# Kernel optimization log

Measured on AMD Instinct MI355X. Metric: run time of the kernel, lower is better.

The kernel has to match this reference:

```python
import jax, jax.numpy as jnp
import numpy as np

N_NODES = 20000
N_EDGES = 320000
N_GRAPHS = 512
HEADS1 = 10
C1 = 78   # per-head out channels of gcn1
C2 = 100  # out channels of gcn2 (heads=1)
NEG_SLOPE = 0.2


def setup_inputs() -> dict:
    key = jax.random.key(0)
    ks = jax.random.split(key, 16)
    glorot = lambda k, shp: jax.random.normal(k, shp, jnp.float32) * np.sqrt(2.0 / (shp[0] + shp[-1]))
    x = jax.random.normal(ks[0], (N_NODES, 78), jnp.float32)
    edge_index = jax.random.randint(ks[1], (2, N_EDGES), 0, N_NODES, jnp.int64)
    batch = jnp.sort(jax.random.randint(ks[2], (N_NODES,), 0, N_GRAPHS, jnp.int64))
    return {
        "x": x,
        "edge_index": edge_index,
        "batch": batch,
        "num_graphs": N_GRAPHS,
        "W1": glorot(ks[3], (78, HEADS1 * C1)),
        "a_src1": glorot(ks[4], (HEADS1, C1)),
        "a_dst1": glorot(ks[5], (HEADS1, C1)),
        "b1": jnp.zeros((HEADS1 * C1,), jnp.float32),
        "W2": glorot(ks[6], (HEADS1 * C1, C2)),
        "a_src2": glorot(ks[7], (1, C2)),
        "a_dst2": glorot(ks[8], (1, C2)),
        "b2": jnp.zeros((C2,), jnp.float32),
        "Wg": glorot(ks[9], (C2, C2)),
        "bg": jnp.zeros((C2,), jnp.float32),
    }


def gat_conv(x, src, dst, W, a_src, a_dst, b, heads, out_ch):
    """PyG-style GATConv (concat=True, add_self_loops already applied, eval mode)."""
    N = x.shape[0]
    h = (x @ W).reshape(N, heads, out_ch)          # [N,H,C]
    alpha_s = jnp.einsum('nhc,hc->nh', h, a_src)   # [N,H]
    alpha_d = jnp.einsum('nhc,hc->nh', h, a_dst)
    e = jax.nn.leaky_relu(alpha_s[src] + alpha_d[dst], NEG_SLOPE)  # [E,H]
    # segment softmax over destination nodes
    m = jax.ops.segment_max(e, dst, num_segments=N)                # [N,H]
    e = jnp.exp(e - m[dst])
    denom = jax.ops.segment_sum(e, dst, num_segments=N)
    alpha = e / (denom[dst] + 1e-16)                               # [E,H]
    out = jax.ops.segment_sum(h[src] * alpha[:, :, None], dst, num_segments=N)
    return out.reshape(N, heads * out_ch) + b


def reference(x, edge_index, batch, num_graphs, W1, a_src1, a_dst1, b1,
              W2, a_src2, a_dst2, b2, Wg, bg):
    N = x.shape[0]
    # add self loops (PyG GATConv default)
    loops = jnp.arange(N, dtype=edge_index.dtype)
    src = jnp.concatenate([edge_index[0], loops])
    dst = jnp.concatenate([edge_index[1], loops])
    h = gat_conv(x, src, dst, W1, a_src1, a_dst1, b1, HEADS1, C1)   # [N,780]
    h = jax.nn.elu(h)
    h = gat_conv(h, src, dst, W2, a_src2, a_dst2, b2, 1, C2)        # [N,100]
    h = jax.nn.relu(h)
    g = jax.ops.segment_max(h, batch, num_segments=num_graphs)      # [G,100] global max pool
    g = jax.nn.relu(g @ Wg + bg)
    return g
```

## Files before the change

kernel.cpp:

```cpp
#include <hip/hip_runtime.h>
#include <hip/hip_bf16.h>

#define N_NODES  20000
#define N_EDGES  320000
#define E_TOT    (N_EDGES + N_NODES)
#define N_GRAPHS 512
#define H1 10
#define C1 78
#define F1 780
#define C2 100
#define NEG_SLOPE 0.2f
#define KSPLIT 5
#define K1PAD 96
#define K2PAD 800
#define K2CHUNK 160
#define AP1 104
#define AP2 40
#define HP 12

typedef short bf16x8 __attribute__((ext_vector_type(8)));
typedef float f32x4 __attribute__((ext_vector_type(4)));
typedef unsigned short ushort_t;

__device__ __forceinline__ float bf_lo(unsigned int u) { return __uint_as_float(u << 16); }
__device__ __forceinline__ float bf_hi(unsigned int u) { return __uint_as_float(u & 0xFFFF0000u); }
__device__ __forceinline__ ushort_t f2b(float v) {
  __hip_bfloat16 b = __float2bfloat16(v);
  return *reinterpret_cast<ushort_t*>(&b);
}
__device__ __forceinline__ float lrelu(float v) { return (v > 0.f) ? v : NEG_SLOPE * v; }


__global__ void k_count(const int* __restrict__ ei, int* __restrict__ cnt) {
  int e = blockIdx.x * blockDim.x + threadIdx.x;
  if (e >= E_TOT) return;
  int dst = (e < N_EDGES) ? ei[N_EDGES + e] : (e - N_EDGES);
  atomicAdd(&cnt[dst], 1);
}

__global__ __launch_bounds__(1024) void k_scan(const int* __restrict__ cnt,
                                               int* __restrict__ offs, int n) {
  const int PER = 20;
  int t = threadIdx.x;
  int lane = t & 63, wv = t >> 6;
  int base = t * PER;
  int loc[PER];
  int run = 0;
#pragma unroll
  for (int k = 0; k < PER; k++) {
    int idx = base + k;
    int v = (idx < n) ? cnt[idx] : 0;
    run += v;
    loc[k] = run;
  }
  int total = run;
  int sc = total;
#pragma unroll
  for (int o = 1; o < 64; o <<= 1) {
    int u = __shfl_up(sc, o);
    if (lane >= o) sc += u;
  }
  __shared__ int ws[16];
  if (lane == 63) ws[wv] = sc;
  __syncthreads();
  if (t == 0) {
    int r = 0;
#pragma unroll
    for (int i = 0; i < 16; i++) { int v = ws[i]; ws[i] = r; r += v; }
  }
  __syncthreads();
  int excl = ws[wv] + sc - total;
#pragma unroll
  for (int k = 0; k < PER; k++) {
    int idx = base + k;
    if (idx < n) offs[idx + 1] = excl + loc[k];
  }
  if (t == 0) offs[0] = 0;
}

__global__ void k_scatter(const int* __restrict__ ei, const int* __restrict__ offs,
                          int* __restrict__ cursor, int* __restrict__ srcs,
                          int* __restrict__ dsts) {
  int e = blockIdx.x * blockDim.x + threadIdx.x;
  if (e >= E_TOT) return;
  int src, dst;
  if (e < N_EDGES) { src = ei[e]; dst = ei[N_EDGES + e]; }
  else             { src = dst = e - N_EDGES; }
  int pos = offs[dst] + atomicAdd(&cursor[dst], 1);
  srcs[pos] = src;
  dsts[pos] = dst;
}


#define PR0 (2 * H1 * C1)
#define PR1 (H1 * 80 * K1PAD)
#define PR2 (112 * K2PAD)
#define PR3 (N_NODES * (K2PAD - F1))
#define PR4 (N_NODES * 40)

__global__ void k_prep(const float* __restrict__ W1, const float* __restrict__ a_src,
                       const float* __restrict__ a_dst, const float* __restrict__ W2,
                       const float* __restrict__ x,
                       float* __restrict__ Vs, float* __restrict__ Vd,
                       ushort_t* __restrict__ W1t, ushort_t* __restrict__ W2t,
                       ushort_t* __restrict__ hab, ushort_t* __restrict__ xbf) {
  int t = blockIdx.x * blockDim.x + threadIdx.x;
  if (t < PR0) {
    int which = (t >= H1 * C1) ? 1 : 0;
    int r = t - which * H1 * C1;
    int h = r / C1, k = r - h * C1;
    const float* a = which ? a_dst : a_src;
    float s = 0.f;
    for (int c = 0; c < C1; c++) s += W1[(size_t)k * F1 + h * C1 + c] * a[h * C1 + c];
    (which ? Vd : Vs)[h * C1 + k] = s;
    return;
  }
  t -= PR0;
  if (t < PR1) {
    int h = t / (80 * K1PAD);
    int rem = t - h * 80 * K1PAD;
    int c = rem / K1PAD, k = rem - c * K1PAD;
    float v = (c < C1 && k < C1) ? W1[(size_t)k * F1 + h * C1 + c] : 0.f;
    W1t[t] = f2b(v);
    return;
  }
  t -= PR1;
  if (t < PR2) {
    int c = t / K2PAD, k = t - c * K2PAD;
    float v = (c < C2 && k < F1) ? W2[(size_t)k * C2 + c] : 0.f;
    W2t[t] = f2b(v);
    return;
  }
  t -= PR2;
  if (t < PR3) {
    int n = t / (K2PAD - F1), j = t - n * (K2PAD - F1);
    hab[(size_t)n * K2PAD + F1 + j] = 0;
    return;
  }
  t -= PR3;
  if (t < PR4) {
    int n = t / 40, c2 = t - n * 40;
    ushort2 o;
    if (c2 < 39) { o.x = f2b(x[(size_t)n * C1 + 2 * c2]); o.y = f2b(x[(size_t)n * C1 + 2 * c2 + 1]); }
    else         { o.x = 0; o.y = 0; }
    *(ushort2*)(xbf + (size_t)n * 80 + 2 * c2) = o;
  }
}


__global__ __launch_bounds__(256) void k_alpha1x(const float* __restrict__ x,
                                                 const float* __restrict__ Vs,
                                                 const float* __restrict__ Vd,
                                                 float* __restrict__ asb,
                                                 float* __restrict__ adb) {
  __shared__ float sVs[H1 * C1], sVd[H1 * C1];
  for (int i = threadIdx.x; i < H1 * C1; i += 256) { sVs[i] = Vs[i]; sVd[i] = Vd[i]; }
  __syncthreads();
  int t = blockIdx.x * 256 + threadIdx.x;
  if (t >= N_NODES * H1) return;
  int n = t / H1, h = t - n * H1;
  const float2* row = (const float2*)(x + (size_t)n * C1);
  const float2* vs2 = (const float2*)(sVs + h * C1);
  const float2* vd2 = (const float2*)(sVd + h * C1);
  float s0 = 0.f, s1 = 0.f;
#pragma unroll 13
  for (int i = 0; i < C1 / 2; i++) {
    float2 v = row[i];
    float2 a = vs2[i];
    float2 b = vd2[i];
    s0 += v.x * a.x + v.y * a.y;
    s1 += v.x * b.x + v.y * b.y;
  }
  asb[(size_t)n * HP + h] = s0;
  adb[(size_t)n * HP + h] = s1;
}


__global__ void k_ex1(const float* __restrict__ asb, const float* __restrict__ adb,
                      const int* __restrict__ srcs, const int* __restrict__ dsts,
                      unsigned int* __restrict__ ex1) {
  int e = blockIdx.x * blockDim.x + threadIdx.x;
  if (e > E_TOT) return;
  unsigned int* o = ex1 + (size_t)e * 5;
  if (e == E_TOT) {
#pragma unroll
    for (int q = 0; q < 5; q++) o[q] = 0u;
    return;
  }
  int s = srcs[e], d = dsts[e];
  const float* pa = asb + (size_t)s * HP;
  const float* pd = adb + (size_t)d * HP;
  float4 a0 = *(const float4*)pa, a1 = *(const float4*)(pa + 4);
  float2 a2 = *(const float2*)(pa + 8);
  float4 d0 = *(const float4*)pd, d1 = *(const float4*)(pd + 4);
  float2 d2 = *(const float2*)(pd + 8);
  float r[10];
  r[0] = __expf(lrelu(a0.x + d0.x)); r[1] = __expf(lrelu(a0.y + d0.y));
  r[2] = __expf(lrelu(a0.z + d0.z)); r[3] = __expf(lrelu(a0.w + d0.w));
  r[4] = __expf(lrelu(a1.x + d1.x)); r[5] = __expf(lrelu(a1.y + d1.y));
  r[6] = __expf(lrelu(a1.z + d1.z)); r[7] = __expf(lrelu(a1.w + d1.w));
  r[8] = __expf(lrelu(a2.x + d2.x)); r[9] = __expf(lrelu(a2.y + d2.y));
#pragma unroll
  for (int q = 0; q < 5; q++)
    o[q] = (unsigned int)f2b(r[2 * q]) | ((unsigned int)f2b(r[2 * q + 1]) << 16);
}


__global__ __launch_bounds__(256) void k_aggv4(const ushort_t* __restrict__ xbf,
                                               const unsigned int* __restrict__ ex1,
                                               const int* __restrict__ offs,
                                               const int* __restrict__ srcs,
                                               ushort_t* __restrict__ xb) {
  int wid = (blockIdx.x * 256 + threadIdx.x) >> 6;
  int lane = threadIdx.x & 63;
  if (wid >= N_NODES) return;
  int n = wid;
  int beg = offs[n], deg = offs[n + 1] - beg;

  float acc[H1][2] = {};
  float sum[H1] = {};

  for (int j = 0; j < deg; j += 2) {
    int e0 = beg + j;
    int s0 = srcs[e0];
    bool v1 = (j + 1) < deg;
    int e1 = v1 ? e0 + 1 : E_TOT;
    int s1 = v1 ? srcs[e0 + 1] : s0;
    unsigned int w0[5], w1[5];
#pragma unroll
    for (int q = 0; q < 5; q++) { w0[q] = ex1[(size_t)e0 * 5 + q]; w1[q] = ex1[(size_t)e1 * 5 + q]; }
    unsigned int xv0 = 0, xv1 = 0;
    if (lane < 39) {
      xv0 = *(const unsigned int*)(xbf + (size_t)s0 * 80 + 2 * lane);
      xv1 = *(const unsigned int*)(xbf + (size_t)s1 * 80 + 2 * lane);
    }
    float xl0 = bf_lo(xv0), xh0 = bf_hi(xv0);
    float xl1 = bf_lo(xv1), xh1 = bf_hi(xv1);
#pragma unroll
    for (int h = 0; h < H1; h++) {
      float p0 = (h & 1) ? bf_hi(w0[h >> 1]) : bf_lo(w0[h >> 1]);
      float p1 = (h & 1) ? bf_hi(w1[h >> 1]) : bf_lo(w1[h >> 1]);
      acc[h][0] += p0 * xl0 + p1 * xl1;
      acc[h][1] += p0 * xh0 + p1 * xh1;
      sum[h] += p0 + p1;
    }
  }

  if (lane < 48) {
    int colu = (lane < 39) ? 2 * lane : C1 + 2 * (lane - 39);
#pragma unroll
    for (int h = 0; h < H1; h++) {
      float iv = 1.f / (sum[h] + 1e-16f);
      ushort2 o;
      if (lane < 39) { o.x = f2b(acc[h][0] * iv); o.y = f2b(acc[h][1] * iv); }
      else           { o.x = 0; o.y = 0; }
      *(ushort2*)(xb + ((size_t)h * N_NODES + n) * K1PAD + colu) = o;
    }
  }
}


__global__ __launch_bounds__(256) void k_bgemm_m(const ushort_t* __restrict__ xb,
                                                 const ushort_t* __restrict__ W1t,
                                                 const float* __restrict__ b1,
                                                 ushort_t* __restrict__ hab) {
  __shared__ ushort_t sA[64 * AP1];
  __shared__ ushort_t sB[80 * AP1];
  int h = blockIdx.y;
  int m0 = blockIdx.x * 64;
  int tid = threadIdx.x;

  for (int i = tid; i < 64 * 12; i += 256) {
    int r = i / 12, cx = i - r * 12;
    uint4 v = make_uint4(0, 0, 0, 0);
    int m = m0 + r;
    if (m < N_NODES) v = *(const uint4*)(xb + ((size_t)h * N_NODES + m) * K1PAD + cx * 8);
    *(uint4*)(sA + r * AP1 + cx * 8) = v;
  }
  for (int i = tid; i < 80 * 12; i += 256) {
    int c = i / 12, cx = i - c * 12;
    uint4 v = *(const uint4*)(W1t + ((size_t)h * 80 + c) * K1PAD + cx * 8);
    *(uint4*)(sB + c * AP1 + cx * 8) = v;
  }
  __syncthreads();

  int w = tid >> 6, l = tid & 63;
  int rb = l & 15, g = l >> 4;
  f32x4 acc[5] = {};
  const ushort_t* pa = sA + (w * 16 + rb) * AP1 + g * 8;
#pragma unroll
  for (int k0 = 0; k0 < K1PAD; k0 += 32) {
    bf16x8 a = *(const bf16x8*)(pa + k0);
#pragma unroll
    for (int ct = 0; ct < 5; ct++) {
      bf16x8 b = *(const bf16x8*)(sB + (ct * 16 + rb) * AP1 + k0 + g * 8);
      acc[ct] = __builtin_amdgcn_mfma_f32_16x16x32_bf16(a, b, acc[ct], 0, 0, 0);
    }
  }

  int mrow = m0 + w * 16 + g * 4;
#pragma unroll
  for (int ct = 0; ct < 5; ct++) {
    int col = ct * 16 + rb;
    if (col >= C1) continue;
    float bias = b1[h * C1 + col];
#pragma unroll
    for (int r = 0; r < 4; r++) {
      int m = mrow + r;
      if (m >= N_NODES) continue;
      float v = acc[ct][r] + bias;
      v = (v > 0.f) ? v : (__expf(v) - 1.f);
      hab[(size_t)m * K2PAD + h * C1 + col] = f2b(v);
    }
  }
}


__global__ __launch_bounds__(256) void k_gemm2m(const ushort_t* __restrict__ hab,
                                                const ushort_t* __restrict__ W2t,
                                                float* __restrict__ part) {
  __shared__ ushort_t sA[64 * AP2];
  __shared__ ushort_t sB[112 * AP2];
  int m0 = blockIdx.x * 64;
  int kz = blockIdx.y * K2CHUNK;
  int tid = threadIdx.x;
  int w = tid >> 6, l = tid & 63;
  int rb = l & 15, g = l >> 4;
  f32x4 acc[7] = {};

  for (int ks = 0; ks < K2CHUNK; ks += 32) {
    int kbase = kz + ks;
    {
      int r = tid >> 2, cx = tid & 3;
      uint4 v = make_uint4(0, 0, 0, 0);
      int m = m0 + r;
      if (m < N_NODES) v = *(const uint4*)(hab + (size_t)m * K2PAD + kbase + cx * 8);
      *(uint4*)(sA + r * AP2 + cx * 8) = v;
    }
    for (int i = tid; i < 112 * 4; i += 256) {
      int c = i >> 2, cx = i & 3;
      uint4 v = *(const uint4*)(W2t + (size_t)c * K2PAD + kbase + cx * 8);
      *(uint4*)(sB + c * AP2 + cx * 8) = v;
    }
    __syncthreads();
    bf16x8 a = *(const bf16x8*)(sA + (w * 16 + rb) * AP2 + g * 8);
#pragma unroll
    for (int ct = 0; ct < 7; ct++) {
      bf16x8 b = *(const bf16x8*)(sB + (ct * 16 + rb) * AP2 + g * 8);
      acc[ct] = __builtin_amdgcn_mfma_f32_16x16x32_bf16(a, b, acc[ct], 0, 0, 0);
    }
    __syncthreads();
  }

  float* P = part + (size_t)blockIdx.y * N_NODES * C2;
  int mrow = m0 + w * 16 + g * 4;
#pragma unroll
  for (int ct = 0; ct < 7; ct++) {
    int col = ct * 16 + rb;
    if (col >= C2) continue;
#pragma unroll
    for (int r = 0; r < 4; r++) {
      int m = mrow + r;
      if (m < N_NODES) P[(size_t)m * C2 + col] = acc[ct][r];
    }
  }
}


__global__ __launch_bounds__(256) void k_redalpha(const float* __restrict__ part,
                                                  const float* __restrict__ a_src,
                                                  const float* __restrict__ a_dst,
                                                  ushort_t* __restrict__ z2b,
                                                  float* __restrict__ as2,
                                                  float* __restrict__ ad2) {
  int wid = (blockIdx.x * 256 + threadIdx.x) >> 6;
  int lane = threadIdx.x & 63;
  if (wid >= N_NODES) return;
  float ps = 0.f, pd = 0.f;
  if (lane < C2 / 2) {
    float2 s = make_float2(0.f, 0.f);
#pragma unroll
    for (int c = 0; c < KSPLIT; c++) {
      float2 v = *(const float2*)(part + (size_t)c * N_NODES * C2 + (size_t)wid * C2 + 2 * lane);
      s.x += v.x; s.y += v.y;
    }
    ushort2 o; o.x = f2b(s.x); o.y = f2b(s.y);
    *(ushort2*)(z2b + (size_t)wid * C2 + 2 * lane) = o;
    ps = s.x * a_src[2 * lane] + s.y * a_src[2 * lane + 1];
    pd = s.x * a_dst[2 * lane] + s.y * a_dst[2 * lane + 1];
  }
#pragma unroll
  for (int o = 32; o; o >>= 1) { ps += __shfl_xor(ps, o); pd += __shfl_xor(pd, o); }
  if (lane == 0) { as2[wid] = ps; ad2[wid] = pd; }
}


__global__ void k_ex2(const float* __restrict__ as2, const float* __restrict__ ad2,
                      const int* __restrict__ srcs, const int* __restrict__ dsts,
                      float* __restrict__ ex2) {
  int e = blockIdx.x * blockDim.x + threadIdx.x;
  if (e > E_TOT) return;
  if (e == E_TOT) { ex2[e] = 0.f; return; }
  float v = as2[srcs[e]] + ad2[dsts[e]];
  ex2[e] = __expf(lrelu(v));
}


__global__ __launch_bounds__(256) void k_gat2v3(const ushort_t* __restrict__ z2b,
                                                const float* __restrict__ ex2,
                                                const int* __restrict__ offs,
                                                const int* __restrict__ srcs,
                                                const float* __restrict__ b2,
                                                const int* __restrict__ batch,
                                                unsigned int* __restrict__ pool) {
  int wid = (blockIdx.x * 256 + threadIdx.x) >> 6;
  int lane = threadIdx.x & 63;
  if (wid >= N_NODES) return;
  int n = wid;
  int beg = offs[n], deg = offs[n + 1] - beg;
  const unsigned int* zrow = (const unsigned int*)z2b;

  float acc0 = 0.f, acc1 = 0.f, sum = 0.f;

  for (int j = 0; j < deg; j += 8) {
    int ej[8], sj[8];
#pragma unroll
    for (int q = 0; q < 8; q++) {
      int jj = j + q;
      bool v = jj < deg;
      ej[q] = v ? beg + jj : E_TOT;
      sj[q] = srcs[v ? beg + jj : beg];
    }
    float p[8];
#pragma unroll
    for (int q = 0; q < 8; q++) p[q] = ex2[ej[q]];
    unsigned int z[8] = {0, 0, 0, 0, 0, 0, 0, 0};
    if (lane < C2 / 2) {
#pragma unroll
      for (int q = 0; q < 8; q++) z[q] = zrow[(size_t)sj[q] * (C2 / 2) + lane];
    }
#pragma unroll
    for (int q = 0; q < 8; q++) {
      acc0 += p[q] * bf_lo(z[q]);
      acc1 += p[q] * bf_hi(z[q]);
      sum += p[q];
    }
  }

  if (lane < C2 / 2) {
    float iv = 1.f / (sum + 1e-16f);
    float v0 = fmaxf(acc0 * iv + b2[2 * lane], 0.f);
    float v1 = fmaxf(acc1 * iv + b2[2 * lane + 1], 0.f);
    int g = batch[n];
    atomicMax(&pool[g * C2 + 2 * lane], __float_as_uint(v0));
    atomicMax(&pool[g * C2 + 2 * lane + 1], __float_as_uint(v1));
  }
}


__global__ __launch_bounds__(128) void k_head(const float* __restrict__ pool,
                                              const float* __restrict__ Wg,
                                              const float* __restrict__ bg,
                                              float* __restrict__ out) {
  __shared__ float row[C2];
  int g = blockIdx.x;
  if (threadIdx.x < C2) row[threadIdx.x] = pool[g * C2 + threadIdx.x];
  __syncthreads();
  int c = threadIdx.x;
  if (c < C2) {
    float acc = bg[c];
    for (int k = 0; k < C2; k++) acc += row[k] * Wg[k * C2 + c];
    out[g * C2 + c] = fmaxf(acc, 0.f);
  }
}


extern "C" void kernel_launch(void* const* d_in, const int* in_sizes, int n_in,
                              void* d_out, int out_size, void* d_ws, size_t ws_size,
                              hipStream_t stream) {
  const float* x      = (const float*)d_in[0];
  const int*   ei     = (const int*)d_in[1];
  const int*   batch  = (const int*)d_in[2];
  const float* W1     = (const float*)d_in[4];
  const float* a_src1 = (const float*)d_in[5];
  const float* a_dst1 = (const float*)d_in[6];
  const float* b1     = (const float*)d_in[7];
  const float* W2     = (const float*)d_in[8];
  const float* a_src2 = (const float*)d_in[9];
  const float* a_dst2 = (const float*)d_in[10];
  const float* b2     = (const float*)d_in[11];
  const float* Wg     = (const float*)d_in[12];
  const float* bg     = (const float*)d_in[13];
  float* out = (float*)d_out;

  char* w = (char*)d_ws;
  size_t off = 0;
  auto alloc = [&](size_t bytes) -> void* {
    void* p = w + off;
    off += (bytes + 255) & ~(size_t)255;
    return p;
  };

  ushort_t* xb  = (ushort_t*)alloc((size_t)H1 * N_NODES * K1PAD * 2);
  ushort_t* hab = (ushort_t*)alloc((size_t)N_NODES * K2PAD * 2);
  float* part   = (float*)alloc((size_t)KSPLIT * N_NODES * C2 * 4);
  float* asb    = (float*)alloc((size_t)N_NODES * HP * 4);
  float* adb    = (float*)alloc((size_t)N_NODES * HP * 4);
  unsigned int* ex1 = (unsigned int*)alloc((size_t)(E_TOT + 1) * 5 * 4);
  ushort_t* xbf = (ushort_t*)alloc((size_t)N_NODES * 80 * 2);
  float* Vs     = (float*)alloc((size_t)H1 * C1 * 4);
  float* Vd     = (float*)alloc((size_t)H1 * C1 * 4);
  ushort_t* W1t = (ushort_t*)alloc((size_t)H1 * 80 * K1PAD * 2);
  ushort_t* W2t = (ushort_t*)alloc((size_t)112 * K2PAD * 2);
  int* cnt           = (int*)alloc((size_t)N_NODES * 4);
  int* cursor        = (int*)alloc((size_t)N_NODES * 4);
  unsigned int* pool = (unsigned int*)alloc((size_t)N_GRAPHS * C2 * 4);
  size_t zspan = (size_t)((char*)(pool + (size_t)N_GRAPHS * C2) - (char*)cnt);
  int* offs   = (int*)alloc((size_t)(N_NODES + 1) * 4);
  int* srcs   = (int*)alloc((size_t)E_TOT * 4);
  int* dsts   = (int*)alloc((size_t)E_TOT * 4);

  float* as2    = (float*)xb;
  float* ad2    = as2 + N_NODES;
  ushort_t* z2b = (ushort_t*)(ad2 + N_NODES);
  float* ex2    = (float*)(z2b + (size_t)N_NODES * C2);

  hipMemsetAsync(cnt, 0, zspan, stream);

  k_count<<<(E_TOT + 255) / 256, 256, 0, stream>>>(ei, cnt);
  k_scan<<<1, 1024, 0, stream>>>(cnt, offs, N_NODES);
  k_scatter<<<(E_TOT + 255) / 256, 256, 0, stream>>>(ei, offs, cursor, srcs, dsts);

  k_prep<<<(PR0 + PR1 + PR2 + PR3 + PR4 + 255) / 256, 256, 0, stream>>>(
      W1, a_src1, a_dst1, W2, x, Vs, Vd, W1t, W2t, hab, xbf);
  k_alpha1x<<<(N_NODES * H1 + 255) / 256, 256, 0, stream>>>(x, Vs, Vd, asb, adb);
  k_ex1<<<(E_TOT + 1 + 255) / 256, 256, 0, stream>>>(asb, adb, srcs, dsts, ex1);
  k_aggv4<<<(N_NODES + 3) / 4, 256, 0, stream>>>(xbf, ex1, offs, srcs, xb);
  k_bgemm_m<<<dim3((N_NODES + 63) / 64, H1), 256, 0, stream>>>(xb, W1t, b1, hab);

  k_gemm2m<<<dim3((N_NODES + 63) / 64, KSPLIT), 256, 0, stream>>>(hab, W2t, part);
  k_redalpha<<<(N_NODES + 3) / 4, 256, 0, stream>>>(part, a_src2, a_dst2, z2b, as2, ad2);
  k_ex2<<<(E_TOT + 1 + 255) / 256, 256, 0, stream>>>(as2, ad2, srcs, dsts, ex2);
  k_gat2v3<<<(N_NODES + 3) / 4, 256, 0, stream>>>(z2b, ex2, offs, srcs, b2, batch, pool);
  k_head<<<N_GRAPHS, 128, 0, stream>>>((const float*)pool, Wg, bg, out);
}
```

Baseline: 280.8 us.

## Use fp16 packed dot2 and head-major edge weights in layer-1 aggregation

Layer-1 aggregation now stores node features and per-edge exp scores in fp16 instead of bf16. The exp scores move to a head-major [H, E] layout so each head's weights for an edge pair load as one aligned 32-bit word. The inner loop uses v_dot2_f32_f16 (fdot2) to accumulate two edges per instruction for the weighted sums and the normaliser, with bitmasks handling odd edge-range boundaries. This replaces the scalar bf16-unpack and FMA work and the padded sentinel edge. It trades bf16 range for fp16 range on unnormalised exp values, so large logits could overflow to inf, and inf multiplied by a zero mask gives NaN.

After: 275.6 us. About the same (-1.8%).

```diff
diff --git a/kernel.cpp b/kernel.cpp
--- a/kernel.cpp
+++ b/kernel.cpp
@@ -20,6 +20,7 @@
 
 typedef short bf16x8 __attribute__((ext_vector_type(8)));
 typedef float f32x4 __attribute__((ext_vector_type(4)));
+typedef _Float16 half2v __attribute__((ext_vector_type(2)));
 typedef unsigned short ushort_t;
 
 __device__ __forceinline__ float bf_lo(unsigned int u) { return __uint_as_float(u << 16); }
@@ -28,7 +29,16 @@
   __hip_bfloat16 b = __float2bfloat16(v);
   return *reinterpret_cast<ushort_t*>(&b);
 }
+__device__ __forceinline__ ushort_t f2h(float v) {
+  _Float16 h = (_Float16)v;
+  return *reinterpret_cast<ushort_t*>(&h);
+}
 __device__ __forceinline__ float lrelu(float v) { return (v > 0.f) ? v : NEG_SLOPE * v; }
+__device__ __forceinline__ float dot2h(unsigned int a, unsigned int b, float c) {
+  union { unsigned int u; half2v v; } A, B;
+  A.u = a; B.u = b;
+  return __builtin_amdgcn_fdot2(A.v, B.v, c, false);
+}
 
 
 __global__ void k_count(const int* __restrict__ ei, int* __restrict__ cnt) {
@@ -103,7 +113,7 @@
                        const float* __restrict__ x,
                        float* __restrict__ Vs, float* __restrict__ Vd,
                        ushort_t* __restrict__ W1t, ushort_t* __restrict__ W2t,
-                       ushort_t* __restrict__ hab, ushort_t* __restrict__ xbf) {
+                       ushort_t* __restrict__ hab, ushort_t* __restrict__ xhf) {
   int t = blockIdx.x * blockDim.x + threadIdx.x;
   if (t < PR0) {
     int which = (t >= H1 * C1) ? 1 : 0;
@@ -141,9 +151,9 @@
   if (t < PR4) {
     int n = t / 40, c2 = t - n * 40;
     ushort2 o;
-    if (c2 < 39) { o.x = f2b(x[(size_t)n * C1 + 2 * c2]); o.y = f2b(x[(size_t)n * C1 + 2 * c2 + 1]); }
+    if (c2 < 39) { o.x = f2h(x[(size_t)n * C1 + 2 * c2]); o.y = f2h(x[(size_t)n * C1 + 2 * c2 + 1]); }
     else         { o.x = 0; o.y = 0; }
-    *(ushort2*)(xbf + (size_t)n * 80 + 2 * c2) = o;
+    *(ushort2*)(xhf + (size_t)n * 80 + 2 * c2) = o;
   }
 }
 
@@ -178,15 +188,9 @@
 
 __global__ void k_ex1(const float* __restrict__ asb, const float* __restrict__ adb,
                       const int* __restrict__ srcs, const int* __restrict__ dsts,
-                      unsigned int* __restrict__ ex1) {
+                      ushort_t* __restrict__ ex1t) {
   int e = blockIdx.x * blockDim.x + threadIdx.x;
-  if (e > E_TOT) return;
-  unsigned int* o = ex1 + (size_t)e * 5;
-  if (e == E_TOT) {
-#pragma unroll
-    for (int q = 0; q < 5; q++) o[q] = 0u;
-    return;
-  }
+  if (e >= E_TOT) return;
   int s = srcs[e], d = dsts[e];
   const float* pa = asb + (size_t)s * HP;
   const float* pd = adb + (size_t)d * HP;
@@ -201,13 +205,12 @@
   r[6] = __expf(lrelu(a1.z + d1.z)); r[7] = __expf(lrelu(a1.w + d1.w));
   r[8] = __expf(lrelu(a2.x + d2.x)); r[9] = __expf(lrelu(a2.y + d2.y));
 #pragma unroll
-  for (int q = 0; q < 5; q++)
-    o[q] = (unsigned int)f2b(r[2 * q]) | ((unsigned int)f2b(r[2 * q + 1]) << 16);
-}
-
-
-__global__ __launch_bounds__(256) void k_aggv4(const ushort_t* __restrict__ xbf,
-                                               const unsigned int* __restrict__ ex1,
+  for (int h = 0; h < H1; h++) ex1t[(size_t)h * E_TOT + e] = f2h(r[h]);
+}
+
+
+__global__ __launch_bounds__(256) void k_aggv5(const ushort_t* __restrict__ xhf,
+                                               const ushort_t* __restrict__ ex1t,
                                                const int* __restrict__ offs,
                                                const int* __restrict__ srcs,
                                                ushort_t* __restrict__ xb) {
@@ -215,34 +218,34 @@
   int lane = threadIdx.x & 63;
   if (wid >= N_NODES) return;
   int n = wid;
-  int beg = offs[n], deg = offs[n + 1] - beg;
-
-  float acc[H1][2] = {};
-  float sum[H1] = {};
-
-  for (int j = 0; j < deg; j += 2) {
-    int e0 = beg + j;
-    int s0 = srcs[e0];
-    bool v1 = (j + 1) < deg;
-    int e1 = v1 ? e0 + 1 : E_TOT;
-    int s1 = v1 ? srcs[e0 + 1] : s0;
-    unsigned int w0[5], w1[5];
-#pragma unroll
-    for (int q = 0; q < 5; q++) { w0[q] = ex1[(size_t)e0 * 5 + q]; w1[q] = ex1[(size_t)e1 * 5 + q]; }
+  int beg = __builtin_amdgcn_readfirstlane(offs[n]);
+  int end = __builtin_amdgcn_readfirstlane(offs[n + 1]);
+
+  float acc0[H1] = {}, acc1[H1] = {}, sum[H1] = {};
+  const unsigned int ONES = 0x3C003C00u;
+
+  for (int e0 = beg & ~1; e0 < end; e0 += 2) {
+    unsigned int m = 0xFFFFFFFFu;
+    if (e0 < beg) m &= 0xFFFF0000u;
+    if (e0 + 1 >= end) m &= 0x0000FFFFu;
+    int s0 = srcs[e0], s1 = srcs[e0 + 1];
+    unsigned int w[H1];
+#pragma unroll
+    for (int h = 0; h < H1; h++)
+      w[h] = *(const unsigned int*)(ex1t + (size_t)h * E_TOT + e0);
     unsigned int xv0 = 0, xv1 = 0;
     if (lane < 39) {
-      xv0 = *(const unsigned int*)(xbf + (size_t)s0 * 80 + 2 * lane);
-      xv1 = *(const unsigned int*)(xbf + (size_t)s1 * 80 + 2 * lane);
-    }
-    float xl0 = bf_lo(xv0), xh0 = bf_hi(xv0);
-    float xl1 = bf_lo(xv1), xh1 = bf_hi(xv1);
+      xv0 = *(const unsigned int*)(xhf + (size_t)s0 * 80 + 2 * lane);
+      xv1 = *(const unsigned int*)(xhf + (size_t)s1 * 80 + 2 * lane);
+    }
+    unsigned int xA = __builtin_amdgcn_perm(xv1, xv0, 0x05040100u) & m;
+    unsigned int xB = __builtin_amdgcn_perm(xv1, xv0, 0x07060302u) & m;
+    unsigned int on = ONES & m;
 #pragma unroll
     for (int h = 0; h < H1; h++) {
-      float p0 = (h & 1) ? bf_hi(w0[h >> 1]) : bf_lo(w0[h >> 1]);
-      float p1 = (h & 1) ? bf_hi(w1[h >> 1]) : bf_lo(w1[h >> 1]);
-      acc[h][0] += p0 * xl0 + p1 * xl1;
-      acc[h][1] += p0 * xh0 + p1 * xh1;
-      sum[h] += p0 + p1;
+      acc0[h] = dot2h(w[h], xA, acc0[h]);
+      acc1[h] = dot2h(w[h], xB, acc1[h]);
+      sum[h]  = dot2h(w[h], on, sum[h]);
     }
   }
 
@@ -252,7 +255,7 @@
     for (int h = 0; h < H1; h++) {
       float iv = 1.f / (sum[h] + 1e-16f);
       ushort2 o;
-      if (lane < 39) { o.x = f2b(acc[h][0] * iv); o.y = f2b(acc[h][1] * iv); }
+      if (lane < 39) { o.x = f2b(acc0[h] * iv); o.y = f2b(acc1[h] * iv); }
       else           { o.x = 0; o.y = 0; }
       *(ushort2*)(xb + ((size_t)h * N_NODES + n) * K1PAD + colu) = o;
     }
@@ -501,17 +504,17 @@
     return p;
   };
 
-  ushort_t* xb  = (ushort_t*)alloc((size_t)H1 * N_NODES * K1PAD * 2);
-  ushort_t* hab = (ushort_t*)alloc((size_t)N_NODES * K2PAD * 2);
-  float* part   = (float*)alloc((size_t)KSPLIT * N_NODES * C2 * 4);
-  float* asb    = (float*)alloc((size_t)N_NODES * HP * 4);
-  float* adb    = (float*)alloc((size_t)N_NODES * HP * 4);
-  unsigned int* ex1 = (unsigned int*)alloc((size_t)(E_TOT + 1) * 5 * 4);
-  ushort_t* xbf = (ushort_t*)alloc((size_t)N_NODES * 80 * 2);
-  float* Vs     = (float*)alloc((size_t)H1 * C1 * 4);
-  float* Vd     = (float*)alloc((size_t)H1 * C1 * 4);
-  ushort_t* W1t = (ushort_t*)alloc((size_t)H1 * 80 * K1PAD * 2);
-  ushort_t* W2t = (ushort_t*)alloc((size_t)112 * K2PAD * 2);
+  ushort_t* xb   = (ushort_t*)alloc((size_t)H1 * N_NODES * K1PAD * 2);
+  ushort_t* hab  = (ushort_t*)alloc((size_t)N_NODES * K2PAD * 2);
+  float* part    = (float*)alloc((size_t)KSPLIT * N_NODES * C2 * 4);
+  float* asb     = (float*)alloc((size_t)N_NODES * HP * 4);
+  float* adb     = (float*)alloc((size_t)N_NODES * HP * 4);
+  ushort_t* ex1t = (ushort_t*)alloc((size_t)H1 * E_TOT * 2);
+  ushort_t* xhf  = (ushort_t*)alloc((size_t)N_NODES * 80 * 2);
+  float* Vs      = (float*)alloc((size_t)H1 * C1 * 4);
+  float* Vd      = (float*)alloc((size_t)H1 * C1 * 4);
+  ushort_t* W1t  = (ushort_t*)alloc((size_t)H1 * 80 * K1PAD * 2);
+  ushort_t* W2t  = (ushort_t*)alloc((size_t)112 * K2PAD * 2);
   int* cnt           = (int*)alloc((size_t)N_NODES * 4);
   int* cursor        = (int*)alloc((size_t)N_NODES * 4);
   unsigned int* pool = (unsigned int*)alloc((size_t)N_GRAPHS * C2 * 4);
@@ -532,10 +535,10 @@
   k_scatter<<<(E_TOT + 255) / 256, 256, 0, stream>>>(ei, offs, cursor, srcs, dsts);
 
   k_prep<<<(PR0 + PR1 + PR2 + PR3 + PR4 + 255) / 256, 256, 0, stream>>>(
-      W1, a_src1, a_dst1, W2, x, Vs, Vd, W1t, W2t, hab, xbf);
+      W1, a_src1, a_dst1, W2, x, Vs, Vd, W1t, W2t, hab, xhf);
   k_alpha1x<<<(N_NODES * H1 + 255) / 256, 256, 0, stream>>>(x, Vs, Vd, asb, adb);
-  k_ex1<<<(E_TOT + 1 + 255) / 256, 256, 0, stream>>>(asb, adb, srcs, dsts, ex1);
-  k_aggv4<<<(N_NODES + 3) / 4, 256, 0, stream>>>(xbf, ex1, offs, srcs, xb);
+  k_ex1<<<(E_TOT + 255) / 256, 256, 0, stream>>>(asb, adb, srcs, dsts, ex1t);
+  k_aggv5<<<(N_NODES + 3) / 4, 256, 0, stream>>>(xhf, ex1t, offs, srcs, xb);
   k_bgemm_m<<<dim3((N_NODES + 63) / 64, H1), 256, 0, stream>>>(xb, W1t, b1, hab);
 
   k_gemm2m<<<dim3((N_NODES + 63) / 64, KSPLIT), 256, 0, stream>>>(hab, W2t, part);
```
